# Performance work log

Measured on AMD Instinct MI355X. Metric: run time of the kernel, lower is better.

The kernel has to match this reference:

```python
import jax, jax.numpy as jnp
import numpy as np

N, D, E, L, H, F1, G, A = 4096, 256, 131072, 3, 4, 128, 16, 32

def setup_inputs() -> dict:
    key = jax.random.key(0)
    ks = jax.random.split(key, 12)
    s = lambda k, shape, fan: jax.random.normal(k, shape, jnp.float32) / np.sqrt(fan)
    return {
        "x": jax.random.normal(ks[0], (N, D), jnp.float32),
        "edge_attr": jax.random.uniform(ks[1], (E,), jnp.float32),
        "conv_Wself": s(ks[2], (L, D, D), D),
        "conv_Wnbr": s(ks[3], (L, D, D), D),
        "conv_b": jnp.zeros((L, D), jnp.float32),
        "bn_gamma": jnp.ones((L - 1, D), jnp.float32),
        "bn_beta": jnp.zeros((L - 1, D), jnp.float32),
        "bn_mean": jnp.zeros((L - 1, D), jnp.float32),
        "bn_var": jnp.ones((L - 1, D), jnp.float32),
        "Wqkv": s(ks[4], (3, D, D), D),
        "bqkv": jnp.zeros((3, D), jnp.float32),
        "Wo": s(ks[5], (D, D), D),
        "bo": jnp.zeros((D,), jnp.float32),
        "fc1_W": s(ks[6], (D, F1), D),
        "fc1_b": jnp.zeros((F1,), jnp.float32),
        "AW1": s(ks[7], (G, F1, A), F1),
        "Ab1": jnp.zeros((G, A), jnp.float32),
        "AW2": s(ks[8], (G, A, 1), A),
        "Ab2": jnp.zeros((G, 1), jnp.float32),
        "edge_index": jax.random.randint(ks[9], (2, E), 0, N, jnp.int32),
        "node_groups": jax.random.randint(ks[10], (N,), 0, G, jnp.int32),
    }


def reference(x, edge_attr, conv_Wself, conv_Wnbr, conv_b, bn_gamma, bn_beta,
              bn_mean, bn_var, Wqkv, bqkv, Wo, bo, fc1_W, fc1_b,
              AW1, Ab1, AW2, Ab2, edge_index, node_groups):
    src, dst = edge_index[0], edge_index[1]
    # message-passing conv stack (edge_attr only used by the last, non-attention layer)
    for i in range(L):
        msg = x[src]
        if i == L - 1:
            msg = msg * edge_attr[:, None]
        agg = jax.ops.segment_sum(msg, dst, num_segments=N)
        x = x @ conv_Wself[i] + agg @ conv_Wnbr[i] + conv_b[i]
        if i < L - 1:
            x = bn_gamma[i] * (x - bn_mean[i]) * jax.lax.rsqrt(bn_var[i] + 1e-5) + bn_beta[i]
            x = jax.nn.elu(x)
    # hierarchy self-attention over all N nodes (batch of 1), residual add
    dh = D // H
    q = (x @ Wqkv[0] + bqkv[0]).reshape(N, H, dh)
    k = (x @ Wqkv[1] + bqkv[1]).reshape(N, H, dh)
    v = (x @ Wqkv[2] + bqkv[2]).reshape(N, H, dh)
    scores = jnp.einsum('nhd,mhd->hnm', q, k) / np.sqrt(dh).astype(np.float32)
    attn = jax.nn.softmax(scores, axis=-1)
    o = jnp.einsum('hnm,mhd->nhd', attn, v).reshape(N, D) @ Wo + bo
    x = x + o
    feats = jax.nn.elu(x @ fc1_W + fc1_b)  # [N, F1]; dropout is eval no-op
    # MoE-style per-node group adapter routing: gather tiny MLP weights per node
    h = jax.nn.relu(jnp.einsum('nd,nda->na', feats, AW1[node_groups]) + Ab1[node_groups])
    out = jnp.einsum('na,nao->no', h, AW2[node_groups]) + Ab2[node_groups]  # [N, 1]
    return out
```

## Files before the change

### kernel.cpp

```cpp
#include <hip/hip_runtime.h>
#include <math.h>

#define NN   4096
#define DIM  256
#define NE   131072
#define NH   4
#define DH   64
#define F1D  128
#define NG   16
#define AD   32

typedef unsigned short u16;
typedef unsigned int   u32;
typedef _Float16 f16;
typedef __attribute__((ext_vector_type(8))) _Float16 half8;
typedef __attribute__((ext_vector_type(4))) float f32x4;

#define MFMA16(a, b, c) __builtin_amdgcn_mfma_f32_16x16x32_f16(a, b, c, 0, 0, 0)

__device__ inline u16 f2h(float x) { union { f16 f; u16 u; } c; c.f = (f16)x; return c.u; }
__device__ inline float h2f(u16 h) { union { f16 f; u16 u; } c; c.u = h; return (float)c.f; }
__device__ inline void split16(float x, u16& h, u16& l) {
    union { f16 f; u16 u; } ch, cl;
    ch.f = (f16)x;
    cl.f = (f16)(x - (float)ch.f);
    h = ch.u; l = cl.u;
}
__device__ inline int swz64(int row, int colByte) {
    return row * 64 + ((colByte ^ ((row & 7) << 4)) >> 1);
}

__global__ void csr_count(const int* __restrict__ dst, int* __restrict__ cnt) {
    int e = blockIdx.x * 256 + threadIdx.x;
    atomicAdd(&cnt[dst[e]], 1);
}

__global__ __launch_bounds__(1024) void csr_scan(
    int* __restrict__ cnt, int* __restrict__ off)
{
    __shared__ int wsum[16];
    const int t = threadIdx.x;
    const int lane = t & 63;
    int4 v = *(const int4*)&cnt[t * 4];
    const int s = v.x + v.y + v.z + v.w;
    int acc = s;
    #pragma unroll
    for (int o = 1; o < 64; o <<= 1) {
        int u = __shfl_up(acc, o);
        if (lane >= o) acc += u;
    }
    if (lane == 63) wsum[t >> 6] = acc;
    __syncthreads();
    if (t < 16) {
        int w0 = wsum[t];
        int a2 = w0;
        #pragma unroll
        for (int o = 1; o < 16; o <<= 1) {
            int u = __shfl_up(a2, o);
            if (t >= o) a2 += u;
        }
        wsum[t] = a2 - w0;
    }
    __syncthreads();
    const int base = wsum[t >> 6] + (acc - s);
    off[t * 4 + 0] = base;
    off[t * 4 + 1] = base + v.x;
    off[t * 4 + 2] = base + v.x + v.y;
    off[t * 4 + 3] = base + v.x + v.y + v.z;
    *(int4*)&cnt[t * 4] = make_int4(0, 0, 0, 0);
    if (t == 1023) off[NN] = base + s;
}

__global__ void csr_fill(const int* __restrict__ dst, const int* __restrict__ src,
                         const float* __restrict__ eattr, const int* __restrict__ off,
                         int* __restrict__ cur, int* __restrict__ esrc,
                         float* __restrict__ ewt) {
    int e = blockIdx.x * 256 + threadIdx.x;
    int d = dst[e];
    int pos = off[d] + atomicAdd(&cur[d], 1);
    esrc[pos] = src[e];
    ewt[pos]  = eattr[e];
}

__global__ __launch_bounds__(256) void prep_kernel(
    const float* __restrict__ x,
    const float* __restrict__ Ws, const float* __restrict__ Wn,
    const float* __restrict__ Wqkv, const float* __restrict__ Wo,
    const float* __restrict__ fc1W,
    u16* __restrict__ xh, u16* __restrict__ xl,
    u16* __restrict__ wch, u16* __restrict__ wcl,
    u16* __restrict__ w4h, u16* __restrict__ w4l,
    u16* __restrict__ f1h, u16* __restrict__ f1l,
    int* __restrict__ cur)
{
    const int b = blockIdx.x;
    const int t = threadIdx.x;
    if (b < 1024) {
        const int gid = b * 256 + t;
        const float4 v = *(const float4*)&x[(size_t)gid * 4];
        u16 h[4], l[4];
        split16(v.x, h[0], l[0]); split16(v.y, h[1], l[1]);
        split16(v.z, h[2], l[2]); split16(v.w, h[3], l[3]);
        *(uint2*)&xh[(size_t)gid * 4] =
            make_uint2((u32)h[0] | ((u32)h[1] << 16), (u32)h[2] | ((u32)h[3] << 16));
        *(uint2*)&xl[(size_t)gid * 4] =
            make_uint2((u32)l[0] | ((u32)l[1] << 16), (u32)l[2] | ((u32)l[3] << 16));
    } else if (b < 1408) {
        const int gid = (b - 1024) * 256 + t;
        const int L = gid / 32768;
        const int rem = gid % 32768;
        const int m = rem / 128;
        const int k4 = (rem % 128) * 4;
        const float* S = Ws + (size_t)L * 65536;
        const float* Nb = Wn + (size_t)L * 65536;
        u16 h[4], l[4];
        #pragma unroll
        for (int j = 0; j < 4; ++j) {
            const int k = k4 + j;
            const float v = (k < 256) ? S[(size_t)k * 256 + m]
                                      : Nb[(size_t)(k - 256) * 256 + m];
            split16(v, h[j], l[j]);
        }
        const size_t o = (size_t)L * 131072 + (size_t)m * 512 + k4;
        *(uint2*)&wch[o] = make_uint2((u32)h[0] | ((u32)h[1] << 16), (u32)h[2] | ((u32)h[3] << 16));
        *(uint2*)&wcl[o] = make_uint2((u32)l[0] | ((u32)l[1] << 16), (u32)l[2] | ((u32)l[3] << 16));
    } else if (b < 1664) {
        const int gid = (b - 1408) * 256 + t;
        const int mat = gid / 16384;
        const int rem = gid % 16384;
        const int m = rem / 64;
        const int k4 = (rem % 64) * 4;
        const float* W = (mat < 3) ? Wqkv + (size_t)mat * 65536 : Wo;
        u16 h[4], l[4];
        #pragma unroll
        for (int j = 0; j < 4; ++j)
            split16(W[(size_t)(k4 + j) * 256 + m], h[j], l[j]);
        const size_t o = (size_t)mat * 65536 + (size_t)m * 256 + k4;
        *(uint2*)&w4h[o] = make_uint2((u32)h[0] | ((u32)h[1] << 16), (u32)h[2] | ((u32)h[3] << 16));
        *(uint2*)&w4l[o] = make_uint2((u32)l[0] | ((u32)l[1] << 16), (u32)l[2] | ((u32)l[3] << 16));
    } else if (b < 1696) {
        const int gid = (b - 1664) * 256 + t;
        const int m = gid / 64;
        const int k4 = (gid % 64) * 4;
        u16 h[4], l[4];
        #pragma unroll
        for (int j = 0; j < 4; ++j)
            split16(fc1W[(size_t)(k4 + j) * F1D + m], h[j], l[j]);
        const size_t o = (size_t)m * 256 + k4;
        *(uint2*)&f1h[o] = make_uint2((u32)h[0] | ((u32)h[1] << 16), (u32)h[2] | ((u32)h[3] << 16));
        *(uint2*)&f1l[o] = make_uint2((u32)l[0] | ((u32)l[1] << 16), (u32)l[2] | ((u32)l[3] << 16));
    } else {
        const int gid = (b - 1696) * 256 + t;
        if (gid < NN / 4) *(int4*)&cur[gid * 4] = make_int4(0, 0, 0, 0);
    }
}

template<bool LAST>
__global__ __launch_bounds__(256) void agg_kernel(
    const float* __restrict__ x, const int* __restrict__ esrc,
    const float* __restrict__ ewt, const int* __restrict__ off,
    u16* __restrict__ aggh, u16* __restrict__ aggl)
{
    const int node = blockIdx.x * 4 + (threadIdx.x >> 6);
    const int lane = threadIdx.x & 63;
    const int d4 = lane * 4;
    int j = off[node];
    const int j1 = off[node + 1];
    float4 acc = make_float4(0.f, 0.f, 0.f, 0.f);
    for (; j + 4 <= j1; j += 4) {
        const int s0 = esrc[j], s1 = esrc[j + 1], s2 = esrc[j + 2], s3 = esrc[j + 3];
        const float4 x0 = *(const float4*)&x[(size_t)s0 * DIM + d4];
        const float4 x1 = *(const float4*)&x[(size_t)s1 * DIM + d4];
        const float4 x2 = *(const float4*)&x[(size_t)s2 * DIM + d4];
        const float4 x3 = *(const float4*)&x[(size_t)s3 * DIM + d4];
        const float w0 = LAST ? ewt[j]     : 1.f;
        const float w1 = LAST ? ewt[j + 1] : 1.f;
        const float w2 = LAST ? ewt[j + 2] : 1.f;
        const float w3 = LAST ? ewt[j + 3] : 1.f;
        acc.x = fmaf(x0.x, w0, acc.x); acc.y = fmaf(x0.y, w0, acc.y);
        acc.z = fmaf(x0.z, w0, acc.z); acc.w = fmaf(x0.w, w0, acc.w);
        acc.x = fmaf(x1.x, w1, acc.x); acc.y = fmaf(x1.y, w1, acc.y);
        acc.z = fmaf(x1.z, w1, acc.z); acc.w = fmaf(x1.w, w1, acc.w);
        acc.x = fmaf(x2.x, w2, acc.x); acc.y = fmaf(x2.y, w2, acc.y);
        acc.z = fmaf(x2.z, w2, acc.z); acc.w = fmaf(x2.w, w2, acc.w);
        acc.x = fmaf(x3.x, w3, acc.x); acc.y = fmaf(x3.y, w3, acc.y);
        acc.z = fmaf(x3.z, w3, acc.z); acc.w = fmaf(x3.w, w3, acc.w);
    }
    for (; j < j1; ++j) {
        const int s = esrc[j];
        const float w = LAST ? ewt[j] : 1.f;
        const float4 xv = *(const float4*)&x[(size_t)s * DIM + d4];
        acc.x = fmaf(xv.x, w, acc.x); acc.y = fmaf(xv.y, w, acc.y);
        acc.z = fmaf(xv.z, w, acc.z); acc.w = fmaf(xv.w, w, acc.w);
    }
    u16 h[4], l[4];
    split16(acc.x, h[0], l[0]); split16(acc.y, h[1], l[1]);
    split16(acc.z, h[2], l[2]); split16(acc.w, h[3], l[3]);
    *(uint2*)&aggh[(size_t)node * DIM + d4] =
        make_uint2((u32)h[0] | ((u32)h[1] << 16), (u32)h[2] | ((u32)h[3] << 16));
    *(uint2*)&aggl[(size_t)node * DIM + d4] =
        make_uint2((u32)l[0] | ((u32)l[1] << 16), (u32)l[2] | ((u32)l[3] << 16));
}

template<int EPI>
__global__ __launch_bounds__(256) void conv_mfma(
    const u16* __restrict__ xh, const u16* __restrict__ xl,
    const u16* __restrict__ gh, const u16* __restrict__ gl,
    const u16* __restrict__ bth, const u16* __restrict__ btl,
    const float* __restrict__ bias,
    const float* __restrict__ gamma, const float* __restrict__ beta,
    const float* __restrict__ bnmean, const float* __restrict__ bnvar,
    float* __restrict__ outf, u16* __restrict__ oh, u16* __restrict__ ol)
{
    __shared__ u16 lds[13824];
    u16* As_h = lds;
    u16* As_l = lds + 2304;
    u16* Bs_h = lds + 4608;
    u16* Bs_l = lds + 9216;
    #define TKP 72

    const int tid  = threadIdx.x;
    const int row0 = blockIdx.y * 32;
    const int col0 = blockIdx.x * 64;

    const int w   = tid >> 6;
    const int l15 = tid & 15, h4 = (tid & 63) >> 4;
    const int rh  = w & 1, ch = w >> 1;
    const int arow = tid >> 3, acs = (tid & 7) * 8;
    const int brow = tid & 63, bseg = tid >> 6;
    const int bc = bseg * 16;

    uint4 sah, sal, sbh0, sbh1, sbl0, sbl1;
    {
        sah = *((const uint4*)&xh[(size_t)(row0 + arow) * DIM + acs]);
        sal = *((const uint4*)&xl[(size_t)(row0 + arow) * DIM + acs]);
        const u16* pbh = bth + (size_t)(col0 + brow) * 512 + bc;
        const u16* pbl = btl + (size_t)(col0 + brow) * 512 + bc;
        sbh0 = ((const uint4*)pbh)[0]; sbh1 = ((const uint4*)pbh)[1];
        sbl0 = ((const uint4*)pbl)[0]; sbl1 = ((const uint4*)pbl)[1];
    }

    const f32x4 z4 = {0.f, 0.f, 0.f, 0.f};
    f32x4 acc[2] = {z4, z4};

    for (int kt = 0; kt < 8; ++kt) {
        *(uint4*)&As_h[arow * TKP + acs] = sah;
        *(uint4*)&As_l[arow * TKP + acs] = sal;
        *(uint4*)&Bs_h[brow * TKP + bc]     = sbh0;
        *(uint4*)&Bs_h[brow * TKP + bc + 8] = sbh1;
        *(uint4*)&Bs_l[brow * TKP + bc]     = sbl0;
        *(uint4*)&Bs_l[brow * TKP + bc + 8] = sbl1;
        if (kt + 1 < 8) {
            const int kn = kt + 1;
            const u16 *pah, *pal;
            if (kn < 4) {
                pah = xh + (size_t)(row0 + arow) * DIM + kn * 64 + acs;
                pal = xl + (size_t)(row0 + arow) * DIM + kn * 64 + acs;
            } else {
                pah = gh + (size_t)(row0 + arow) * DIM + (kn - 4) * 64 + acs;
                pal = gl + (size_t)(row0 + arow) * DIM + (kn - 4) * 64 + acs;
            }
            sah = *((const uint4*)pah);
            sal = *((const uint4*)pal);
            const u16* pbh = bth + (size_t)(col0 + brow) * 512 + kn * 64 + bc;
            const u16* pbl = btl + (size_t)(col0 + brow) * 512 + kn * 64 + bc;
            sbh0 = ((const uint4*)pbh)[0]; sbh1 = ((const uint4*)pbh)[1];
            sbl0 = ((const uint4*)pbl)[0]; sbl1 = ((const uint4*)pbl)[1];
        }
        __syncthreads();

        __builtin_amdgcn_s_setprio(1);
        #pragma unroll
        for (int kc = 0; kc < 2; ++kc) {
            const int dc = kc * 32 + h4 * 8;
            half8 afh, afl, bfh[2], bfl[2];
            afh = *(const half8*)&As_h[(rh * 16 + l15) * TKP + dc];
            afl = *(const half8*)&As_l[(rh * 16 + l15) * TKP + dc];
            #pragma unroll
            for (int bb = 0; bb < 2; ++bb) {
                const int r = ch * 32 + bb * 16 + l15;
                bfh[bb] = *(const half8*)&Bs_h[r * TKP + dc];
                bfl[bb] = *(const half8*)&Bs_l[r * TKP + dc];
            }
            #pragma unroll
            for (int bb = 0; bb < 2; ++bb) {
                acc[bb] = MFMA16(afh, bfh[bb], acc[bb]);
                acc[bb] = MFMA16(afh, bfl[bb], acc[bb]);
                acc[bb] = MFMA16(afl, bfh[bb], acc[bb]);
            }
        }
        __builtin_amdgcn_s_setprio(0);
        __syncthreads();
    }

    #pragma unroll
    for (int bb = 0; bb < 2; ++bb) {
        const int c  = col0 + ch * 32 + bb * 16 + l15;
        const int r0 = row0 + rh * 16 + h4 * 4;
        #pragma unroll
        for (int i = 0; i < 4; ++i) {
            const int r = r0 + i;
            float t = acc[bb][i] + bias[c];
            if (EPI == 1) {
                t = gamma[c] * (t - bnmean[c]) * rsqrtf(bnvar[c] + 1e-5f) + beta[c];
                t = t > 0.f ? t : expm1f(t);
            }
            outf[(size_t)r * DIM + c] = t;
            u16 hh, ll;
            split16(t, hh, ll);
            oh[(size_t)r * DIM + c] = hh;
            ol[(size_t)r * DIM + c] = ll;
        }
    }
    #undef TKP
}

__global__ __launch_bounds__(256) void qkv_mfma(
    const u16* __restrict__ xh, const u16* __restrict__ xl,
    const u16* __restrict__ wth, const u16* __restrict__ wtl,
    const float* __restrict__ bias,
    u16* __restrict__ qh_o, u16* __restrict__ ql_o,
    u16* __restrict__ kh_o, u16* __restrict__ kl_o,
    u16* __restrict__ vt_o)
{
    __shared__ u16 lds[4 * 4608];
    u16* As_h = lds;
    u16* As_l = lds + 4608;
    u16* Bs_h = lds + 9216;
    u16* Bs_l = lds + 13824;
    #define TKP 72

    const int tid  = threadIdx.x;
    const int row0 = blockIdx.y * 64;
    const int mat  = blockIdx.x >> 2;
    const int col0 = (blockIdx.x & 3) * 64;
    const float* biasp = bias + mat * DIM;

    const int w   = tid >> 6;
    const int l15 = tid & 15, h4 = (tid & 63) >> 4;
    const int rh  = w & 1, ch = w >> 1;
    const int lrow = tid & 63, lseg = tid >> 6;
    const int lc = lseg * 16;

    const size_t brow = (size_t)(mat * 256 + col0 + lrow) * 256;
    uint4 sah0, sah1, sal0, sal1, sbh0, sbh1, sbl0, sbl1;
    {
        const u16* pah = xh + (size_t)(row0 + lrow) * DIM + lc;
        const u16* pal = xl + (size_t)(row0 + lrow) * DIM + lc;
        sah0 = ((const uint4*)pah)[0]; sah1 = ((const uint4*)pah)[1];
        sal0 = ((const uint4*)pal)[0]; sal1 = ((const uint4*)pal)[1];
        sbh0 = ((const uint4*)(wth + brow + lc))[0]; sbh1 = ((const uint4*)(wth + brow + lc))[1];
        sbl0 = ((const uint4*)(wtl + brow + lc))[0]; sbl1 = ((const uint4*)(wtl + brow + lc))[1];
    }

    const f32x4 z4 = {0.f, 0.f, 0.f, 0.f};
    f32x4 acc[2][2] = {{z4, z4}, {z4, z4}};

    for (int kt = 0; kt < 4; ++kt) {
        *(uint4*)&As_h[lrow * TKP + lc]     = sah0;
        *(uint4*)&As_h[lrow * TKP + lc + 8] = sah1;
        *(uint4*)&As_l[lrow * TKP + lc]     = sal0;
        *(uint4*)&As_l[lrow * TKP + lc + 8] = sal1;
        *(uint4*)&Bs_h[lrow * TKP + lc]     = sbh0;
        *(uint4*)&Bs_h[lrow * TKP + lc + 8] = sbh1;
        *(uint4*)&Bs_l[lrow * TKP + lc]     = sbl0;
        *(uint4*)&Bs_l[lrow * TKP + lc + 8] = sbl1;
        if (kt + 1 < 4) {
            const int kb = (kt + 1) * 64 + lc;
            const u16* pah = xh + (size_t)(row0 + lrow) * DIM + kb;
            const u16* pal = xl + (size_t)(row0 + lrow) * DIM + kb;
            sah0 = ((const uint4*)pah)[0]; sah1 = ((const uint4*)pah)[1];
            sal0 = ((const uint4*)pal)[0]; sal1 = ((const uint4*)pal)[1];
            sbh0 = ((const uint4*)(wth + brow + kb))[0]; sbh1 = ((const uint4*)(wth + brow + kb))[1];
            sbl0 = ((const uint4*)(wtl + brow + kb))[0]; sbl1 = ((const uint4*)(wtl + brow + kb))[1];
        }
        __syncthreads();

        __builtin_amdgcn_s_setprio(1);
        #pragma unroll
        for (int kc = 0; kc < 2; ++kc) {
            const int dc = kc * 32 + h4 * 8;
            half8 afh[2], afl[2], bfh[2], bfl[2];
            #pragma unroll
            for (int ab = 0; ab < 2; ++ab) {
                const int r = rh * 32 + ab * 16 + l15;
                afh[ab] = *(const half8*)&As_h[r * TKP + dc];
                afl[ab] = *(const half8*)&As_l[r * TKP + dc];
            }
            #pragma unroll
            for (int bb = 0; bb < 2; ++bb) {
                const int r = ch * 32 + bb * 16 + l15;
                bfh[bb] = *(const half8*)&Bs_h[r * TKP + dc];
                bfl[bb] = *(const half8*)&Bs_l[r * TKP + dc];
            }
            #pragma unroll
            for (int ab = 0; ab < 2; ++ab)
                #pragma unroll
                for (int bb = 0; bb < 2; ++bb) {
                    acc[ab][bb] = MFMA16(afh[ab], bfh[bb], acc[ab][bb]);
                    acc[ab][bb] = MFMA16(afh[ab], bfl[bb], acc[ab][bb]);
                    acc[ab][bb] = MFMA16(afl[ab], bfh[bb], acc[ab][bb]);
                }
        }
        __builtin_amdgcn_s_setprio(0);
        __syncthreads();
    }

    const float s = (mat == 0) ? 0.125f : 1.0f;
    u16* oph = (mat == 0) ? qh_o : kh_o;
    u16* opl = (mat == 0) ? ql_o : kl_o;
    #pragma unroll
    for (int ab = 0; ab < 2; ++ab)
        #pragma unroll
        for (int bb = 0; bb < 2; ++bb) {
            const int c  = col0 + ch * 32 + bb * 16 + l15;
            const int r0 = row0 + rh * 32 + ab * 16 + h4 * 4;
            if (mat < 2) {
                #pragma unroll
                for (int i = 0; i < 4; ++i) {
                    const int r = r0 + i;
                    const float t = (acc[ab][bb][i] + biasp[c]) * s;
                    u16 hh, ll;
                    split16(t, hh, ll);
                    oph[(size_t)r * DIM + c] = hh;
                    opl[(size_t)r * DIM + c] = ll;
                }
            } else {
                u16 v[4];
                #pragma unroll
                for (int i = 0; i < 4; ++i)
                    v[i] = f2h(acc[ab][bb][i] + biasp[c]);
                *(uint2*)&vt_o[(size_t)c * NN + r0] =
                    make_uint2((u32)v[0] | ((u32)v[1] << 16), (u32)v[2] | ((u32)v[3] << 16));
            }
        }
    #undef TKP
}

__global__ __launch_bounds__(256) void wo_fused(
    const u16* __restrict__ p0, const u16* __restrict__ p1,
    const u16* __restrict__ p2, const u16* __restrict__ p3,
    const float* __restrict__ mp, const float* __restrict__ lp,
    const u16* __restrict__ Bth, const u16* __restrict__ Btl,
    const float* __restrict__ bias, const float* __restrict__ resid,
    u16* __restrict__ outh, u16* __restrict__ outl)
{
    __shared__ u16 lds[13824];
    u16* As_h = lds;
    u16* As_l = lds + 2304;
    u16* Bs_h = lds + 4608;
    u16* Bs_l = lds + 9216;
    #define TKP 72
    const int K = DIM, M = DIM;

    const int tid  = threadIdx.x;
    const int row0 = blockIdx.y * 32;
    const int col0 = blockIdx.x * 64;

    const int w   = tid >> 6;
    const int l15 = tid & 15, h4 = (tid & 63) >> 4;
    const int rh  = w & 1, ch = w >> 1;
    const int arow = tid >> 3, acs = (tid & 7) * 8;
    const int brow = tid & 63, bseg = tid >> 6;
    const int bc = bseg * 16;
    const int r = row0 + arow;

    uint4 pa0, pa1, pa2, pa3, sbh0, sbh1, sbl0, sbl1;
    {
        const size_t ao = (size_t)r * DIM + acs;
        pa0 = *(const uint4*)&p0[ao];
        pa1 = *(const uint4*)&p1[ao];
        pa2 = *(const uint4*)&p2[ao];
        pa3 = *(const uint4*)&p3[ao];
        const u16* pbh = Bth + (size_t)(col0 + brow) * K + bc;
        const u16* pbl = Btl + (size_t)(col0 + brow) * K + bc;
        sbh0 = ((const uint4*)pbh)[0]; sbh1 = ((const uint4*)pbh)[1];
        sbl0 = ((const uint4*)pbl)[0]; sbl1 = ((const uint4*)pbl)[1];
    }

    const f32x4 z4 = {0.f, 0.f, 0.f, 0.f};
    f32x4 acc[2] = {z4, z4};

    for (int kt = 0; kt < 4; ++kt) {
        {
            const int hd = kt;
            const float m0 = mp[((size_t)0 * NN + r) * NH + hd];
            const float m1 = mp[((size_t)1 * NN + r) * NH + hd];
            const float m2 = mp[((size_t)2 * NN + r) * NH + hd];
            const float m3 = mp[((size_t)3 * NN + r) * NH + hd];
            const float M2 = fmaxf(fmaxf(m0, m1), fmaxf(m2, m3));
            const float w0 = lp[((size_t)0 * NN + r) * NH + hd] * __expf(m0 - M2);
            const float w1 = lp[((size_t)1 * NN + r) * NH + hd] * __expf(m1 - M2);
            const float w2 = lp[((size_t)2 * NN + r) * NH + hd] * __expf(m2 - M2);
            const float w3 = lp[((size_t)3 * NN + r) * NH + hd] * __expf(m3 - M2);
            const float inv = 1.f / (((w0 + w1) + (w2 + w3)));
            union { uint4 v; u16 u[8]; } a0, a1, a2, a3, oh_, ol_;
            a0.v = pa0; a1.v = pa1; a2.v = pa2; a3.v = pa3;
            #pragma unroll
            for (int j = 0; j < 8; ++j) {
                const float mv = (w0 * h2f(a0.u[j]) + w1 * h2f(a1.u[j]) +
                                  w2 * h2f(a2.u[j]) + w3 * h2f(a3.u[j])) * inv;
                split16(mv, oh_.u[j], ol_.u[j]);
            }
            *(uint4*)&As_h[arow * TKP + acs] = oh_.v;
            *(uint4*)&As_l[arow * TKP + acs] = ol_.v;
        }
        *(uint4*)&Bs_h[brow * TKP + bc]     = sbh0;
        *(uint4*)&Bs_h[brow * TKP + bc + 8] = sbh1;
        *(uint4*)&Bs_l[brow * TKP + bc]     = sbl0;
        *(uint4*)&Bs_l[brow * TKP + bc + 8] = sbl1;
        if (kt + 1 < 4) {
            const size_t ao = (size_t)r * DIM + (kt + 1) * 64 + acs;
            pa0 = *(const uint4*)&p0[ao];
            pa1 = *(const uint4*)&p1[ao];
            pa2 = *(const uint4*)&p2[ao];
            pa3 = *(const uint4*)&p3[ao];
            const int kb = (kt + 1) * 64;
            const u16* pbh = Bth + (size_t)(col0 + brow) * K + kb + bc;
            const u16* pbl = Btl + (size_t)(col0 + brow) * K + kb + bc;
            sbh0 = ((const uint4*)pbh)[0]; sbh1 = ((const uint4*)pbh)[1];
            sbl0 = ((const uint4*)pbl)[0]; sbl1 = ((const uint4*)pbl)[1];
        }
        __syncthreads();

        __builtin_amdgcn_s_setprio(1);
        #pragma unroll
        for (int kc = 0; kc < 2; ++kc) {
            const int dc = kc * 32 + h4 * 8;
            half8 afh, afl, bfh[2], bfl[2];
            afh = *(const half8*)&As_h[(rh * 16 + l15) * TKP + dc];
            afl = *(const half8*)&As_l[(rh * 16 + l15) * TKP + dc];
            #pragma unroll
            for (int bb = 0; bb < 2; ++bb) {
                const int rr = ch * 32 + bb * 16 + l15;
                bfh[bb] = *(const half8*)&Bs_h[rr * TKP + dc];
                bfl[bb] = *(const half8*)&Bs_l[rr * TKP + dc];
            }
            #pragma unroll
            for (int bb = 0; bb < 2; ++bb) {
                acc[bb] = MFMA16(afh, bfh[bb], acc[bb]);
                acc[bb] = MFMA16(afh, bfl[bb], acc[bb]);
                acc[bb] = MFMA16(afl, bfh[bb], acc[bb]);
            }
        }
        __builtin_amdgcn_s_setprio(0);
        __syncthreads();
    }

    #pragma unroll
    for (int bb = 0; bb < 2; ++bb) {
        const int c  = col0 + ch * 32 + bb * 16 + l15;
        const int r0 = row0 + rh * 16 + h4 * 4;
        #pragma unroll
        for (int i = 0; i < 4; ++i) {
            const int rr = r0 + i;
            float t = acc[bb][i] + bias[c] + resid[(size_t)rr * M + c];
            u16 hh, ll;
            split16(t, hh, ll);
            outh[(size_t)rr * M + c] = hh;
            outl[(size_t)rr * M + c] = ll;
        }
    }
    #undef TKP
}

__global__ __launch_bounds__(256) void fc1_mfma(
    const u16* __restrict__ Ah, const u16* __restrict__ Al,
    const u16* __restrict__ Bth, const u16* __restrict__ Btl,
    const float* __restrict__ bias, float* __restrict__ outf)
{
    __shared__ u16 lds[13824];
    u16* As_h = lds;
    u16* As_l = lds + 2304;
    u16* Bs_h = lds + 4608;
    u16* Bs_l = lds + 9216;
    #define TKP 72
    const int K = DIM, M = F1D;

    const int tid  = threadIdx.x;
    const int row0 = blockIdx.y * 32;
    const int col0 = blockIdx.x * 64;

    const int w   = tid >> 6;
    const int l15 = tid & 15, h4 = (tid & 63) >> 4;
    const int rh  = w & 1, ch = w >> 1;
    const int arow = tid >> 3, acs = (tid & 7) * 8;
    const int brow = tid & 63, bseg = tid >> 6;
    const int bc = bseg * 16;

    uint4 sah, sal, sbh0, sbh1, sbl0, sbl1;
    {
        sah = *((const uint4*)&Ah[(size_t)(row0 + arow) * K + acs]);
        sal = *((const uint4*)&Al[(size_t)(row0 + arow) * K + acs]);
        const u16* pbh = Bth + (size_t)(col0 + brow) * K + bc;
        const u16* pbl = Btl + (size_t)(col0 + brow) * K + bc;
        sbh0 = ((const uint4*)pbh)[0]; sbh1 = ((const uint4*)pbh)[1];
        sbl0 = ((const uint4*)pbl)[0]; sbl1 = ((const uint4*)pbl)[1];
    }

    const f32x4 z4 = {0.f, 0.f, 0.f, 0.f};
    f32x4 acc[2] = {z4, z4};

    for (int kt = 0; kt < 4; ++kt) {
        *(uint4*)&As_h[arow * TKP + acs] = sah;
        *(uint4*)&As_l[arow * TKP + acs] = sal;
        *(uint4*)&Bs_h[brow * TKP + bc]     = sbh0;
        *(uint4*)&Bs_h[brow * TKP + bc + 8] = sbh1;
        *(uint4*)&Bs_l[brow * TKP + bc]     = sbl0;
        *(uint4*)&Bs_l[brow * TKP + bc + 8] = sbl1;
        if (kt + 1 < 4) {
            const int kb = (kt + 1) * 64;
            sah = *((const uint4*)&Ah[(size_t)(row0 + arow) * K + kb + acs]);
            sal = *((const uint4*)&Al[(size_t)(row0 + arow) * K + kb + acs]);
            const u16* pbh = Bth + (size_t)(col0 + brow) * K + kb + bc;
            const u16* pbl = Btl + (size_t)(col0 + brow) * K + kb + bc;
            sbh0 = ((const uint4*)pbh)[0]; sbh1 = ((const uint4*)pbh)[1];
            sbl0 = ((const uint4*)pbl)[0]; sbl1 = ((const uint4*)pbl)[1];
        }
        __syncthreads();

        __builtin_amdgcn_s_setprio(1);
        #pragma unroll
        for (int kc = 0; kc < 2; ++kc) {
            const int dc = kc * 32 + h4 * 8;
            half8 afh, afl, bfh[2], bfl[2];
            afh = *(const half8*)&As_h[(rh * 16 + l15) * TKP + dc];
            afl = *(const half8*)&As_l[(rh * 16 + l15) * TKP + dc];
            #pragma unroll
            for (int bb = 0; bb < 2; ++bb) {
                const int rr = ch * 32 + bb * 16 + l15;
                bfh[bb] = *(const half8*)&Bs_h[rr * TKP + dc];
                bfl[bb] = *(const half8*)&Bs_l[rr * TKP + dc];
            }
            #pragma unroll
            for (int bb = 0; bb < 2; ++bb) {
                acc[bb] = MFMA16(afh, bfh[bb], acc[bb]);
                acc[bb] = MFMA16(afh, bfl[bb], acc[bb]);
                acc[bb] = MFMA16(afl, bfh[bb], acc[bb]);
            }
        }
        __builtin_amdgcn_s_setprio(0);
        __syncthreads();
    }

    #pragma unroll
    for (int bb = 0; bb < 2; ++bb) {
        const int c  = col0 + ch * 32 + bb * 16 + l15;
        const int r0 = row0 + rh * 16 + h4 * 4;
        #pragma unroll
        for (int i = 0; i < 4; ++i) {
            const int rr = r0 + i;
            float t = acc[bb][i] + bias[c];
            t = t > 0.f ? t : expm1f(t);
            outf[(size_t)rr * M + c] = t;
        }
    }
    #undef TKP
}

#define QB 128
#define KB 64
#define NSPLIT 4
#define NKT (NN / KB)

__global__ __launch_bounds__(512, 2) void attn_kernel(
    const u16* __restrict__ qhi, const u16* __restrict__ qlo,
    const u16* __restrict__ khi, const u16* __restrict__ klo,
    const u16* __restrict__ vT,
    u16* __restrict__ op0, u16* __restrict__ op1,
    u16* __restrict__ op2, u16* __restrict__ op3,
    float* __restrict__ mpart, float* __restrict__ lpart)
{
    __shared__ u16 lds[24576];
    u16* Kh0 = lds;
    u16* Kl0 = lds + 4096;
    u16* Vt0 = lds + 8192;
    u16* Kh1 = lds + 12288;
    u16* Kl1 = lds + 16384;
    u16* Vt1 = lds + 20480;
    u16* Qh  = lds;
    u16* Ql  = lds + 8192;

    const int tid = threadIdx.x;
    const int h   = blockIdx.y;
    const int q0  = blockIdx.x * QB;
    const int sp  = blockIdx.z;
    const int kt0 = (sp * NKT) / NSPLIT;
    const int kt1 = ((sp + 1) * NKT) / NSPLIT;

    const int w   = tid >> 6;
    const int l15 = tid & 15, h4 = (tid & 63) >> 4;
    const int lrow = tid & 63, lseg = tid >> 6;
    const int gq8 = h * DH + lseg * 8;

    {
        const int qrow = tid >> 2, qseg = tid & 3;
        const u16* s0 = qhi + (size_t)(q0 + qrow) * DIM + h * DH + qseg * 16;
        const u16* s1 = qlo + (size_t)(q0 + qrow) * DIM + h * DH + qseg * 16;
        uint4 a = ((const uint4*)s0)[0], b = ((const uint4*)s0)[1];
        uint4 c = ((const uint4*)s1)[0], d = ((const uint4*)s1)[1];
        *(uint4*)&Qh[swz64(qrow, qseg * 32)]      = a;
        *(uint4*)&Qh[swz64(qrow, qseg * 32 + 16)] = b;
        *(uint4*)&Ql[swz64(qrow, qseg * 32)]      = c;
        *(uint4*)&Ql[swz64(qrow, qseg * 32 + 16)] = d;
    }

    uint4 rk, rl, rv;
    auto load_tile = [&](int kt_ld) {
        const int key0 = kt_ld * KB;
        rk = *(const uint4*)(khi + (size_t)(key0 + lrow) * DIM + gq8);
        rl = *(const uint4*)(klo + (size_t)(key0 + lrow) * DIM + gq8);
        rv = *(const uint4*)(vT + (size_t)(h * DH + lrow) * NN + key0 + lseg * 8);
    };
    load_tile(kt0);
    __syncthreads();

    half8 qf[2][2];
    #pragma unroll
    for (int kc = 0; kc < 2; ++kc) {
        const int r = w * 16 + l15;
        const int cb = kc * 64 + h4 * 16;
        qf[kc][0] = *(const half8*)&Qh[swz64(r, cb)];
        qf[kc][1] = *(const half8*)&Ql[swz64(r, cb)];
    }
    __syncthreads();

    auto stage_to = [&](u16* Kh, u16* Kl, u16* Vt) {
        const int idx = swz64(lrow, lseg * 16);
        *(uint4*)&Kh[idx] = rk;
        *(uint4*)&Kl[idx] = rl;
        *(uint4*)&Vt[idx] = rv;
    };

    stage_to(Kh0, Kl0, Vt0);
    load_tile(kt0 + 1);
    __syncthreads();

    const f32x4 z4 = {0.f, 0.f, 0.f, 0.f};
    f32x4 oacc[4] = {z4, z4, z4, z4};
    float m_run = -3.0e38f, l_run = 0.f;
    const int sl0 = (h4 & 1) * 32 + l15;
    const int sl1 = sl0 + 16;

    auto tile_body = [&](int t, u16* Kc, u16* Lc, u16* Vc,
                         u16* Kn, u16* Ln, u16* Vn) {
        if (t + 1 < kt1) stage_to(Kn, Ln, Vn);
        if (t + 2 < kt1) load_tile(t + 2);

        f32x4 sc[4] = {z4, z4, z4, z4};
        __builtin_amdgcn_s_setprio(1);
        #pragma unroll
        for (int kc = 0; kc < 2; ++kc) {
            const int cb = kc * 64 + h4 * 16;
            half8 kfh[4], kfl[4];
            #pragma unroll
            for (int kcb = 0; kcb < 4; ++kcb) {
                const int r = kcb * 16 + l15;
                const int idx = swz64(r, cb);
                kfh[kcb] = *(const half8*)&Kc[idx];
                kfl[kcb] = *(const half8*)&Lc[idx];
            }
            #pragma unroll
            for (int kcb = 0; kcb < 4; ++kcb) {
                sc[kcb] = MFMA16(kfh[kcb], qf[kc][0], sc[kcb]);
                sc[kcb] = MFMA16(kfl[kcb], qf[kc][0], sc[kcb]);
                sc[kcb] = MFMA16(kfh[kcb], qf[kc][1], sc[kcb]);
            }
        }
        __builtin_amdgcn_s_setprio(0);

        float c0 = fmaxf(fmaxf(sc[0][0], sc[0][1]), fmaxf(sc[0][2], sc[0][3]));
        float c1 = fmaxf(fmaxf(sc[1][0], sc[1][1]), fmaxf(sc[1][2], sc[1][3]));
        float c2 = fmaxf(fmaxf(sc[2][0], sc[2][1]), fmaxf(sc[2][2], sc[2][3]));
        float c3 = fmaxf(fmaxf(sc[3][0], sc[3][1]), fmaxf(sc[3][2], sc[3][3]));
        float pm = fmaxf(fmaxf(c0, c1), fmaxf(c2, c3));
        pm = fmaxf(pm, __shfl_xor(pm, 16));
        pm = fmaxf(pm, __shfl_xor(pm, 32));

        float p[4][4];
        float base, fr = 1.f;
        int resc;
        if (__all(pm - m_run <= 8.f)) {
            base = m_run;
            resc = 0;
        } else {
            const float mnew = fmaxf(m_run, pm);
            fr = __expf(m_run - mnew);
            m_run = mnew;
            base = mnew;
            resc = 1;
        }
        #pragma unroll
        for (int kcb = 0; kcb < 4; ++kcb)
            #pragma unroll
            for (int i = 0; i < 4; ++i)
                p[kcb][i] = __expf(sc[kcb][i] - base);
        float s0s = (p[0][0] + p[0][1]) + (p[0][2] + p[0][3]);
        float s1s = (p[1][0] + p[1][1]) + (p[1][2] + p[1][3]);
        float s2s = (p[2][0] + p[2][1]) + (p[2][2] + p[2][3]);
        float s3s = (p[3][0] + p[3][1]) + (p[3][2] + p[3][3]);
        float ls = (s0s + s1s) + (s2s + s3s);
        ls += __shfl_xor(ls, 16);
        ls += __shfl_xor(ls, 32);
        if (resc) {
            l_run = l_run * fr + ls;
            #pragma unroll
            for (int db = 0; db < 4; ++db) oacc[db] *= fr;
        } else {
            l_run += ls;
        }

        u32 pk01[4], pk23[4];
        #pragma unroll
        for (int kcb = 0; kcb < 4; ++kcb) {
            pk01[kcb] = (u32)f2h(p[kcb][0]) | ((u32)f2h(p[kcb][1]) << 16);
            pk23[kcb] = (u32)f2h(p[kcb][2]) | ((u32)f2h(p[kcb][3]) << 16);
        }

        const int hiSel = h4 >> 1;
        __builtin_amdgcn_s_setprio(1);
        #pragma unroll
        for (int kc = 0; kc < 2; ++kc) {
            const u32 a0 = (u32)__shfl((int)pk01[kc * 2], sl0);
            const u32 a1 = (u32)__shfl((int)pk23[kc * 2], sl0);
            const u32 a2 = (u32)__shfl((int)pk01[kc * 2], sl1);
            const u32 a3 = (u32)__shfl((int)pk23[kc * 2], sl1);
            const u32 b0 = (u32)__shfl((int)pk01[kc * 2 + 1], sl0);
            const u32 b1 = (u32)__shfl((int)pk23[kc * 2 + 1], sl0);
            const u32 b2 = (u32)__shfl((int)pk01[kc * 2 + 1], sl1);
            const u32 b3 = (u32)__shfl((int)pk23[kc * 2 + 1], sl1);
            union { half8 v; u32 u[4]; } pf;
            pf.u[0] = hiSel ? b0 : a0;
            pf.u[1] = hiSel ? b1 : a1;
            pf.u[2] = hiSel ? b2 : a2;
            pf.u[3] = hiSel ? b3 : a3;
            const int cb = kc * 64 + h4 * 16;
            #pragma unroll
            for (int db = 0; db < 4; ++db) {
                const half8 vf = *(const half8*)&Vc[swz64(db * 16 + l15, cb)];
                oacc[db] = MFMA16(vf, pf.v, oacc[db]);
            }
        }
        __builtin_amdgcn_s_setprio(0);
        __syncthreads();
    };

    {
        u16 *Kc = Kh0, *Lc = Kl0, *Vc = Vt0;
        u16 *Kn = Kh1, *Ln = Kl1, *Vn = Vt1;
        for (int t = kt0; t < kt1; ++t) {
            tile_body(t, Kc, Lc, Vc, Kn, Ln, Vn);
            u16* tmp;
            tmp = Kc; Kc = Kn; Kn = tmp;
            tmp = Lc; Lc = Ln; Ln = tmp;
            tmp = Vc; Vc = Vn; Vn = tmp;
        }
    }

    u16* ob = (sp == 0) ? op0 : ((sp == 1) ? op1 : ((sp == 2) ? op2 : op3));
    const float inv = 1.f / l_run;
    #pragma unroll
    for (int db = 0; db < 4; ++db) {
        u32 w0 = (u32)f2h(oacc[db][0] * inv) | ((u32)f2h(oacc[db][1] * inv) << 16);
        u32 w1 = (u32)f2h(oacc[db][2] * inv) | ((u32)f2h(oacc[db][3] * inv) << 16);
        *(uint2*)&ob[(size_t)(q0 + w * 16 + l15) * DIM + h * DH + db * 16 + h4 * 4] =
            make_uint2(w0, w1);
    }
    if (h4 == 0) {
        const int r = w * 16 + l15;
        mpart[((size_t)sp * NN + q0 + r) * NH + h] = m_run;
        lpart[((size_t)sp * NN + q0 + r) * NH + h] = l_run;
    }
}

__global__ __launch_bounds__(256) void adapter_kernel(
    const float* __restrict__ feats, const int* __restrict__ grp,
    const float* __restrict__ AW1, const float* __restrict__ Ab1,
    const float* __restrict__ AW2, const float* __restrict__ Ab2,
    float* __restrict__ out)
{
    const int wv = threadIdx.x >> 6;
    const int n = blockIdx.x * 4 + wv;
    const int lane = threadIdx.x & 63;
    __shared__ float f[4][F1D];
    f[wv][lane]      = feats[(size_t)n * F1D + lane];
    f[wv][lane + 64] = feats[(size_t)n * F1D + 64 + lane];
    const int g = grp[n];
    const float* W1 = AW1 + (size_t)g * F1D * AD;
    const int a = lane & 31;
    const int half = lane >> 5;
    float hsum = 0.f;
    for (int d = 0; d < 64; ++d)
        hsum = fmaf(f[wv][half * 64 + d], W1[(half * 64 + d) * AD + a], hsum);
    hsum += __shfl_xor(hsum, 32);
    hsum = fmaxf(hsum + Ab1[g * AD + a], 0.f);
    float p = hsum * AW2[g * AD + a];
    #pragma unroll
    for (int mm = 1; mm < 32; mm <<= 1) p += __shfl_xor(p, mm);
    if (lane == 0) out[n] = p + Ab2[g];
}

extern "C" void kernel_launch(void* const* d_in, const int* in_sizes, int n_in,
                              void* d_out, int out_size, void* d_ws, size_t ws_size,
                              hipStream_t stream)
{
    const float* x_in   = (const float*)d_in[0];
    const float* eattr  = (const float*)d_in[1];
    const float* Wself  = (const float*)d_in[2];
    const float* Wnbr   = (const float*)d_in[3];
    const float* convb  = (const float*)d_in[4];
    const float* gamma  = (const float*)d_in[5];
    const float* beta   = (const float*)d_in[6];
    const float* bnmean = (const float*)d_in[7];
    const float* bnvar  = (const float*)d_in[8];
    const float* Wqkv   = (const float*)d_in[9];
    const float* bqkv   = (const float*)d_in[10];
    const float* Wo     = (const float*)d_in[11];
    const float* bo     = (const float*)d_in[12];
    const float* fc1W   = (const float*)d_in[13];
    const float* fc1b   = (const float*)d_in[14];
    const float* AW1    = (const float*)d_in[15];
    const float* Ab1    = (const float*)d_in[16];
    const float* AW2    = (const float*)d_in[17];
    const float* Ab2    = (const float*)d_in[18];
    const int*   eidx   = (const int*)d_in[19];
    const int*   grp    = (const int*)d_in[20];
    const int* srcArr = eidx;
    const int* dstArr = eidx + NE;

    float* fws = (float*)d_ws;
    const size_t NM = (size_t)NN * DIM;
    float* bufA  = fws;
    float* bufB  = fws + NM;
    float* bufC  = fws + 2 * NM;
    float* feats = fws + 3 * NM;
    float* mpart = fws + 3 * NM + NM / 2;
    float* lpart = mpart + 4 * NN * NH;
    u16* up = (u16*)(lpart + 4 * NN * NH);
    u16* xpAh = up;             u16* xpAl = xpAh + NM;
    u16* xpBh = xpAl + NM;      u16* xpBl = xpBh + NM;
    u16* aggh = xpBl + NM;      u16* aggl = aggh + NM;
    u16* qh = aggl + NM;        u16* ql = qh + NM;
    u16* kh = ql + NM;          u16* kl = kh + NM;
    u16* vt = kl + NM;
    u16* wcath = vt + NM;
// ... 54 lines not shown
```

Before: 206.5 us.

## Double-buffer LDS in MFMA GEMMs and widen edge-gather unroll to eight

Converts the conv, output-projection and fc1 MFMA GEMM kernels from single-buffered LDS with a register prefetch to double-buffered LDS. Tile k+1 is written to the spare buffer while tile k is being computed, and global loads are issued two tiles ahead, so one barrier per k-step is removed. The aggregation kernel now unrolls the neighbour gather by eight instead of four, putting more independent loads in flight. The cost is twice the LDS per block (about 55 KB), which may reduce occupancy, plus higher register pressure in the gather loop.

Result: no change. 206.2 us (-0.1%).

```diff
diff --git a/kernel.cpp b/kernel.cpp
--- a/kernel.cpp
+++ b/kernel.cpp
@@ -167,24 +167,24 @@
     int j = off[node];
     const int j1 = off[node + 1];
     float4 acc = make_float4(0.f, 0.f, 0.f, 0.f);
-    for (; j + 4 <= j1; j += 4) {
-        const int s0 = esrc[j], s1 = esrc[j + 1], s2 = esrc[j + 2], s3 = esrc[j + 3];
-        const float4 x0 = *(const float4*)&x[(size_t)s0 * DIM + d4];
-        const float4 x1 = *(const float4*)&x[(size_t)s1 * DIM + d4];
-        const float4 x2 = *(const float4*)&x[(size_t)s2 * DIM + d4];
-        const float4 x3 = *(const float4*)&x[(size_t)s3 * DIM + d4];
-        const float w0 = LAST ? ewt[j]     : 1.f;
-        const float w1 = LAST ? ewt[j + 1] : 1.f;
-        const float w2 = LAST ? ewt[j + 2] : 1.f;
-        const float w3 = LAST ? ewt[j + 3] : 1.f;
-        acc.x = fmaf(x0.x, w0, acc.x); acc.y = fmaf(x0.y, w0, acc.y);
-        acc.z = fmaf(x0.z, w0, acc.z); acc.w = fmaf(x0.w, w0, acc.w);
-        acc.x = fmaf(x1.x, w1, acc.x); acc.y = fmaf(x1.y, w1, acc.y);
-        acc.z = fmaf(x1.z, w1, acc.z); acc.w = fmaf(x1.w, w1, acc.w);
-        acc.x = fmaf(x2.x, w2, acc.x); acc.y = fmaf(x2.y, w2, acc.y);
-        acc.z = fmaf(x2.z, w2, acc.z); acc.w = fmaf(x2.w, w2, acc.w);
-        acc.x = fmaf(x3.x, w3, acc.x); acc.y = fmaf(x3.y, w3, acc.y);
-        acc.z = fmaf(x3.z, w3, acc.z); acc.w = fmaf(x3.w, w3, acc.w);
+    for (; j + 8 <= j1; j += 8) {
+        int s[8];
+        #pragma unroll
+        for (int u = 0; u < 8; ++u) s[u] = esrc[j + u];
+        float4 xv[8];
+        #pragma unroll
+        for (int u = 0; u < 8; ++u)
+            xv[u] = *(const float4*)&x[(size_t)s[u] * DIM + d4];
+        float wv[8];
+        #pragma unroll
+        for (int u = 0; u < 8; ++u) wv[u] = LAST ? ewt[j + u] : 1.f;
+        #pragma unroll
+        for (int u = 0; u < 8; ++u) {
+            acc.x = fmaf(xv[u].x, wv[u], acc.x);
+            acc.y = fmaf(xv[u].y, wv[u], acc.y);
+            acc.z = fmaf(xv[u].z, wv[u], acc.z);
+            acc.w = fmaf(xv[u].w, wv[u], acc.w);
+        }
     }
     for (; j < j1; ++j) {
         const int s = esrc[j];
@@ -212,11 +212,7 @@
     const float* __restrict__ bnmean, const float* __restrict__ bnvar,
     float* __restrict__ outf, u16* __restrict__ oh, u16* __restrict__ ol)
 {
-    __shared__ u16 lds[13824];
-    u16* As_h = lds;
-    u16* As_l = lds + 2304;
-    u16* Bs_h = lds + 4608;
-    u16* Bs_l = lds + 9216;
+    __shared__ u16 lds[27648];
     #define TKP 72
 
     const int tid  = threadIdx.x;
@@ -231,56 +227,60 @@
     const int bc = bseg * 16;
 
     uint4 sah, sal, sbh0, sbh1, sbl0, sbl1;
-    {
-        sah = *((const uint4*)&xh[(size_t)(row0 + arow) * DIM + acs]);
-        sal = *((const uint4*)&xl[(size_t)(row0 + arow) * DIM + acs]);
-        const u16* pbh = bth + (size_t)(col0 + brow) * 512 + bc;
-        const u16* pbl = btl + (size_t)(col0 + brow) * 512 + bc;
+    auto load_kt = [&](int kn) {
+        const u16 *pah, *pal;
+        if (kn < 4) {
+            pah = xh + (size_t)(row0 + arow) * DIM + kn * 64 + acs;
+            pal = xl + (size_t)(row0 + arow) * DIM + kn * 64 + acs;
+        } else {
+            pah = gh + (size_t)(row0 + arow) * DIM + (kn - 4) * 64 + acs;
+            pal = gl + (size_t)(row0 + arow) * DIM + (kn - 4) * 64 + acs;
+        }
+        sah = *((const uint4*)pah);
+        sal = *((const uint4*)pal);
+        const u16* pbh = bth + (size_t)(col0 + brow) * 512 + kn * 64 + bc;
+        const u16* pbl = btl + (size_t)(col0 + brow) * 512 + kn * 64 + bc;
         sbh0 = ((const uint4*)pbh)[0]; sbh1 = ((const uint4*)pbh)[1];
         sbl0 = ((const uint4*)pbl)[0]; sbl1 = ((const uint4*)pbl)[1];
-    }
+    };
+    auto stage_to = [&](u16* base) {
+        *(uint4*)&base[arow * TKP + acs]          = sah;
+        *(uint4*)&base[2304 + arow * TKP + acs]   = sal;
+        *(uint4*)&base[4608 + brow * TKP + bc]      = sbh0;
+        *(uint4*)&base[4608 + brow * TKP + bc + 8]  = sbh1;
+        *(uint4*)&base[9216 + brow * TKP + bc]      = sbl0;
+        *(uint4*)&base[9216 + brow * TKP + bc + 8]  = sbl1;
+    };
+
+    load_kt(0);
+    stage_to(lds);
+    load_kt(1);
+    __syncthreads();
 
     const f32x4 z4 = {0.f, 0.f, 0.f, 0.f};
     f32x4 acc[2] = {z4, z4};
 
+    u16* cur = lds;
+    u16* nxt = lds + 13824;
     for (int kt = 0; kt < 8; ++kt) {
-        *(uint4*)&As_h[arow * TKP + acs] = sah;
-        *(uint4*)&As_l[arow * TKP + acs] = sal;
-        *(uint4*)&Bs_h[brow * TKP + bc]     = sbh0;
-        *(uint4*)&Bs_h[brow * TKP + bc + 8] = sbh1;
-        *(uint4*)&Bs_l[brow * TKP + bc]     = sbl0;
-        *(uint4*)&Bs_l[brow * TKP + bc + 8] = sbl1;
-        if (kt + 1 < 8) {
-            const int kn = kt + 1;
-            const u16 *pah, *pal;
-            if (kn < 4) {
-                pah = xh + (size_t)(row0 + arow) * DIM + kn * 64 + acs;
-                pal = xl + (size_t)(row0 + arow) * DIM + kn * 64 + acs;
-            } else {
-                pah = gh + (size_t)(row0 + arow) * DIM + (kn - 4) * 64 + acs;
-                pal = gl + (size_t)(row0 + arow) * DIM + (kn - 4) * 64 + acs;
-            }
-            sah = *((const uint4*)pah);
-            sal = *((const uint4*)pal);
-            const u16* pbh = bth + (size_t)(col0 + brow) * 512 + kn * 64 + bc;
-            const u16* pbl = btl + (size_t)(col0 + brow) * 512 + kn * 64 + bc;
-            sbh0 = ((const uint4*)pbh)[0]; sbh1 = ((const uint4*)pbh)[1];
-            sbl0 = ((const uint4*)pbl)[0]; sbl1 = ((const uint4*)pbl)[1];
-        }
-        __syncthreads();
-
+        if (kt + 1 < 8) stage_to(nxt);
+        if (kt + 2 < 8) load_kt(kt + 2);
+        const u16* Ah_ = cur;
+        const u16* Al_ = cur + 2304;
+        const u16* Bh_ = cur + 4608;
+        const u16* Bl_ = cur + 9216;
         __builtin_amdgcn_s_setprio(1);
         #pragma unroll
         for (int kc = 0; kc < 2; ++kc) {
             const int dc = kc * 32 + h4 * 8;
             half8 afh, afl, bfh[2], bfl[2];
-            afh = *(const half8*)&As_h[(rh * 16 + l15) * TKP + dc];
-            afl = *(const half8*)&As_l[(rh * 16 + l15) * TKP + dc];
+            afh = *(const half8*)&Ah_[(rh * 16 + l15) * TKP + dc];
+            afl = *(const half8*)&Al_[(rh * 16 + l15) * TKP + dc];
             #pragma unroll
             for (int bb = 0; bb < 2; ++bb) {
                 const int r = ch * 32 + bb * 16 + l15;
-                bfh[bb] = *(const half8*)&Bs_h[r * TKP + dc];
-                bfl[bb] = *(const half8*)&Bs_l[r * TKP + dc];
+                bfh[bb] = *(const half8*)&Bh_[r * TKP + dc];
+                bfl[bb] = *(const half8*)&Bl_[r * TKP + dc];
             }
             #pragma unroll
             for (int bb = 0; bb < 2; ++bb) {
@@ -291,6 +291,7 @@
         }
         __builtin_amdgcn_s_setprio(0);
         __syncthreads();
+        u16* t2 = cur; cur = nxt; nxt = t2;
     }
 
     #pragma unroll
@@ -445,11 +446,7 @@
     const float* __restrict__ bias, const float* __restrict__ resid,
     u16* __restrict__ outh, u16* __restrict__ outl)
 {
-    __shared__ u16 lds[13824];
-    u16* As_h = lds;
-    u16* As_l = lds + 2304;
-    u16* Bs_h = lds + 4608;
-    u16* Bs_l = lds + 9216;
+    __shared__ u16 lds[27648];
     #define TKP 72
     const int K = DIM, M = DIM;
 
@@ -466,75 +463,73 @@
     const int r = row0 + arow;
 
     uint4 pa0, pa1, pa2, pa3, sbh0, sbh1, sbl0, sbl1;
-    {
-        const size_t ao = (size_t)r * DIM + acs;
+    auto load_kt = [&](int kn) {
+        const size_t ao = (size_t)r * DIM + kn * 64 + acs;
         pa0 = *(const uint4*)&p0[ao];
         pa1 = *(const uint4*)&p1[ao];
         pa2 = *(const uint4*)&p2[ao];
         pa3 = *(const uint4*)&p3[ao];
-        const u16* pbh = Bth + (size_t)(col0 + brow) * K + bc;
-        const u16* pbl = Btl + (size_t)(col0 + brow) * K + bc;
+        const u16* pbh = Bth + (size_t)(col0 + brow) * K + kn * 64 + bc;
+        const u16* pbl = Btl + (size_t)(col0 + brow) * K + kn * 64 + bc;
         sbh0 = ((const uint4*)pbh)[0]; sbh1 = ((const uint4*)pbh)[1];
         sbl0 = ((const uint4*)pbl)[0]; sbl1 = ((const uint4*)pbl)[1];
-    }
+    };
+    auto stage_to = [&](u16* base, int hd) {
+        const float m0 = mp[((size_t)0 * NN + r) * NH + hd];
+        const float m1 = mp[((size_t)1 * NN + r) * NH + hd];
+        const float m2 = mp[((size_t)2 * NN + r) * NH + hd];
+        const float m3 = mp[((size_t)3 * NN + r) * NH + hd];
+        const float M2 = fmaxf(fmaxf(m0, m1), fmaxf(m2, m3));
+        const float w0 = lp[((size_t)0 * NN + r) * NH + hd] * __expf(m0 - M2);
+        const float w1 = lp[((size_t)1 * NN + r) * NH + hd] * __expf(m1 - M2);
+        const float w2 = lp[((size_t)2 * NN + r) * NH + hd] * __expf(m2 - M2);
+        const float w3 = lp[((size_t)3 * NN + r) * NH + hd] * __expf(m3 - M2);
+        const float inv = 1.f / (((w0 + w1) + (w2 + w3)));
+        union { uint4 v; u16 u[8]; } a0, a1, a2, a3, oh_, ol_;
+        a0.v = pa0; a1.v = pa1; a2.v = pa2; a3.v = pa3;
+        #pragma unroll
+        for (int j = 0; j < 8; ++j) {
+            const float mv = (w0 * h2f(a0.u[j]) + w1 * h2f(a1.u[j]) +
+                              w2 * h2f(a2.u[j]) + w3 * h2f(a3.u[j])) * inv;
+            split16(mv, oh_.u[j], ol_.u[j]);
+        }
+        *(uint4*)&base[arow * TKP + acs]        = oh_.v;
+        *(uint4*)&base[2304 + arow * TKP + acs] = ol_.v;
+        *(uint4*)&base[4608 + brow * TKP + bc]     = sbh0;
+        *(uint4*)&base[4608 + brow * TKP + bc + 8] = sbh1;
+        *(uint4*)&base[9216 + brow * TKP + bc]     = sbl0;
+        *(uint4*)&base[9216 + brow * TKP + bc + 8] = sbl1;
+    };
+
+    load_kt(0);
+    stage_to(lds, 0);
+    load_kt(1);
+    __syncthreads();
 
     const f32x4 z4 = {0.f, 0.f, 0.f, 0.f};
     f32x4 acc[2] = {z4, z4};
 
+    u16* cur = lds;
+    u16* nxt = lds + 13824;
     for (int kt = 0; kt < 4; ++kt) {
-        {
-            const int hd = kt;
-            const float m0 = mp[((size_t)0 * NN + r) * NH + hd];
-            const float m1 = mp[((size_t)1 * NN + r) * NH + hd];
-            const float m2 = mp[((size_t)2 * NN + r) * NH + hd];
-            const float m3 = mp[((size_t)3 * NN + r) * NH + hd];
-            const float M2 = fmaxf(fmaxf(m0, m1), fmaxf(m2, m3));
-            const float w0 = lp[((size_t)0 * NN + r) * NH + hd] * __expf(m0 - M2);
-            const float w1 = lp[((size_t)1 * NN + r) * NH + hd] * __expf(m1 - M2);
-            const float w2 = lp[((size_t)2 * NN + r) * NH + hd] * __expf(m2 - M2);
-            const float w3 = lp[((size_t)3 * NN + r) * NH + hd] * __expf(m3 - M2);
-            const float inv = 1.f / (((w0 + w1) + (w2 + w3)));
-            union { uint4 v; u16 u[8]; } a0, a1, a2, a3, oh_, ol_;
-            a0.v = pa0; a1.v = pa1; a2.v = pa2; a3.v = pa3;
-            #pragma unroll
-            for (int j = 0; j < 8; ++j) {
-                const float mv = (w0 * h2f(a0.u[j]) + w1 * h2f(a1.u[j]) +
-                                  w2 * h2f(a2.u[j]) + w3 * h2f(a3.u[j])) * inv;
-                split16(mv, oh_.u[j], ol_.u[j]);
-            }
-            *(uint4*)&As_h[arow * TKP + acs] = oh_.v;
-            *(uint4*)&As_l[arow * TKP + acs] = ol_.v;
-        }
-        *(uint4*)&Bs_h[brow * TKP + bc]     = sbh0;
-        *(uint4*)&Bs_h[brow * TKP + bc + 8] = sbh1;
-        *(uint4*)&Bs_l[brow * TKP + bc]     = sbl0;
-        *(uint4*)&Bs_l[brow * TKP + bc + 8] = sbl1;
-        if (kt + 1 < 4) {
-            const size_t ao = (size_t)r * DIM + (kt + 1) * 64 + acs;
-            pa0 = *(const uint4*)&p0[ao];
-            pa1 = *(const uint4*)&p1[ao];
-            pa2 = *(const uint4*)&p2[ao];
-            pa3 = *(const uint4*)&p3[ao];
-            const int kb = (kt + 1) * 64;
-            const u16* pbh = Bth + (size_t)(col0 + brow) * K + kb + bc;
-            const u16* pbl = Btl + (size_t)(col0 + brow) * K + kb + bc;
-            sbh0 = ((const uint4*)pbh)[0]; sbh1 = ((const uint4*)pbh)[1];
-            sbl0 = ((const uint4*)pbl)[0]; sbl1 = ((const uint4*)pbl)[1];
-        }
-        __syncthreads();
-
+        if (kt + 1 < 4) stage_to(nxt, kt + 1);
+        if (kt + 2 < 4) load_kt(kt + 2);
+        const u16* Ah_ = cur;
+        const u16* Al_ = cur + 2304;
+        const u16* Bh_ = cur + 4608;
+        const u16* Bl_ = cur + 9216;
         __builtin_amdgcn_s_setprio(1);
         #pragma unroll
         for (int kc = 0; kc < 2; ++kc) {
             const int dc = kc * 32 + h4 * 8;
             half8 afh, afl, bfh[2], bfl[2];
-            afh = *(const half8*)&As_h[(rh * 16 + l15) * TKP + dc];
-            afl = *(const half8*)&As_l[(rh * 16 + l15) * TKP + dc];
+            afh = *(const half8*)&Ah_[(rh * 16 + l15) * TKP + dc];
+            afl = *(const half8*)&Al_[(rh * 16 + l15) * TKP + dc];
             #pragma unroll
             for (int bb = 0; bb < 2; ++bb) {
                 const int rr = ch * 32 + bb * 16 + l15;
-                bfh[bb] = *(const half8*)&Bs_h[rr * TKP + dc];
-                bfl[bb] = *(const half8*)&Bs_l[rr * TKP + dc];
+                bfh[bb] = *(const half8*)&Bh_[rr * TKP + dc];
+                bfl[bb] = *(const half8*)&Bl_[rr * TKP + dc];
             }
             #pragma unroll
             for (int bb = 0; bb < 2; ++bb) {
@@ -545,6 +540,7 @@
         }
         __builtin_amdgcn_s_setprio(0);
         __syncthreads();
+        u16* t2 = cur; cur = nxt; nxt = t2;
     }
 
     #pragma unroll
@@ -569,11 +565,7 @@
     const u16* __restrict__ Bth, const u16* __restrict__ Btl,
     const float* __restrict__ bias, float* __restrict__ outf)
 {
-    __shared__ u16 lds[13824];
-    u16* As_h = lds;
-    u16* As_l = lds + 2304;
-    u16* Bs_h = lds + 4608;
-    u16* Bs_l = lds + 9216;
+    __shared__ u16 lds[27648];
     #define TKP 72
     const int K = DIM, M = F1D;
 
@@ -589,48 +581,52 @@
     const int bc = bseg * 16;
 
     uint4 sah, sal, sbh0, sbh1, sbl0, sbl1;
-    {
-        sah = *((const uint4*)&Ah[(size_t)(row0 + arow) * K + acs]);
-        sal = *((const uint4*)&Al[(size_t)(row0 + arow) * K + acs]);
-        const u16* pbh = Bth + (size_t)(col0 + brow) * K + bc;
-        const u16* pbl = Btl + (size_t)(col0 + brow) * K + bc;
+    auto load_kt = [&](int kn) {
+        sah = *((const uint4*)&Ah[(size_t)(row0 + arow) * K + kn * 64 + acs]);
+        sal = *((const uint4*)&Al[(size_t)(row0 + arow) * K + kn * 64 + acs]);
+        const u16* pbh = Bth + (size_t)(col0 + brow) * K + kn * 64 + bc;
+        const u16* pbl = Btl + (size_t)(col0 + brow) * K + kn * 64 + bc;
         sbh0 = ((const uint4*)pbh)[0]; sbh1 = ((const uint4*)pbh)[1];
         sbl0 = ((const uint4*)pbl)[0]; sbl1 = ((const uint4*)pbl)[1];
-    }
+    };
+    auto stage_to = [&](u16* base) {
+        *(uint4*)&base[arow * TKP + acs]        = sah;
+        *(uint4*)&base[2304 + arow * TKP + acs] = sal;
+        *(uint4*)&base[4608 + brow * TKP + bc]     = sbh0;
+        *(uint4*)&base[4608 + brow * TKP + bc + 8] = sbh1;
+        *(uint4*)&base[9216 + brow * TKP + bc]     = sbl0;
+        *(uint4*)&base[9216 + brow * TKP + bc + 8] = sbl1;
+    };
+
+    load_kt(0);
+    stage_to(lds);
+    load_kt(1);
+    __syncthreads();
 
     const f32x4 z4 = {0.f, 0.f, 0.f, 0.f};
     f32x4 acc[2] = {z4, z4};
 
+    u16* cur = lds;
+    u16* nxt = lds + 13824;
     for (int kt = 0; kt < 4; ++kt) {
-        *(uint4*)&As_h[arow * TKP + acs] = sah;
-        *(uint4*)&As_l[arow * TKP + acs] = sal;
-        *(uint4*)&Bs_h[brow * TKP + bc]     = sbh0;
-        *(uint4*)&Bs_h[brow * TKP + bc + 8] = sbh1;
-        *(uint4*)&Bs_l[brow * TKP + bc]     = sbl0;
-        *(uint4*)&Bs_l[brow * TKP + bc + 8] = sbl1;
-        if (kt + 1 < 4) {
-            const int kb = (kt + 1) * 64;
-            sah = *((const uint4*)&Ah[(size_t)(row0 + arow) * K + kb + acs]);
-            sal = *((const uint4*)&Al[(size_t)(row0 + arow) * K + kb + acs]);
-            const u16* pbh = Bth + (size_t)(col0 + brow) * K + kb + bc;
-            const u16* pbl = Btl + (size_t)(col0 + brow) * K + kb + bc;
-            sbh0 = ((const uint4*)pbh)[0]; sbh1 = ((const uint4*)pbh)[1];
-            sbl0 = ((const uint4*)pbl)[0]; sbl1 = ((const uint4*)pbl)[1];
-        }
-        __syncthreads();
-
+        if (kt + 1 < 4) stage_to(nxt);
+        if (kt + 2 < 4) load_kt(kt + 2);
+        const u16* Ah_ = cur;
+        const u16* Al_ = cur + 2304;
+        const u16* Bh_ = cur + 4608;
+        const u16* Bl_ = cur + 9216;
         __builtin_amdgcn_s_setprio(1);
         #pragma unroll
         for (int kc = 0; kc < 2; ++kc) {
             const int dc = kc * 32 + h4 * 8;
             half8 afh, afl, bfh[2], bfl[2];
-            afh = *(const half8*)&As_h[(rh * 16 + l15) * TKP + dc];
-            afl = *(const half8*)&As_l[(rh * 16 + l15) * TKP + dc];
+            afh = *(const half8*)&Ah_[(rh * 16 + l15) * TKP + dc];
+            afl = *(const half8*)&Al_[(rh * 16 + l15) * TKP + dc];
             #pragma unroll
             for (int bb = 0; bb < 2; ++bb) {
                 const int rr = ch * 32 + bb * 16 + l15;
-                bfh[bb] = *(const half8*)&Bs_h[rr * TKP + dc];
-                bfl[bb] = *(const half8*)&Bs_l[rr * TKP + dc];
+                bfh[bb] = *(const half8*)&Bh_[rr * TKP + dc];
+                bfl[bb] = *(const half8*)&Bl_[rr * TKP + dc];
             }
             #pragma unroll
             for (int bb = 0; bb < 2; ++bb) {
@@ -641,6 +637,7 @@
         }
         __builtin_amdgcn_s_setprio(0);
         __syncthreads();
+        u16* t2 = cur; cur = nxt; nxt = t2;
     }
 
     #pragma unroll
```
